# Kernel tuning notes

Measured on AMD Instinct MI355X. Metric: run time of the kernel, lower is better.

## Reference

```python
import jax, jax.numpy as jnp
import numpy as np

ALPHA = 0.2          # leaky relu negative slope
SCALE_ATT = 1.0
NEG_MASK = -9e15


def setup_inputs() -> dict:
    key = jax.random.key(0)
    k1, k2, k3, k4 = jax.random.split(key, 4)
    B, N, Din, Dout = 32, 1024, 256, 256
    h = jax.random.normal(k1, (B, N, Din), dtype=jnp.float32)
    adj = jax.random.randint(k2, (B, N, N), 0, 2, dtype=jnp.int32)
    W = jax.random.normal(k3, (Dout, Din), dtype=jnp.float32) * (1.0 / np.sqrt(Din))
    b = jnp.zeros((Dout,), dtype=jnp.float32)
    a = jax.random.normal(k4, (2 * Dout,), dtype=jnp.float32) * 0.1
    return {"h": h, "adj": adj, "W": W, "b": b, "a": a}


def reference(h, adj, W, b, a):
    # z: [B, N, Dout]
    z = jnp.einsum('bnd,od->bno', h, W) + b
    Dout = z.shape[-1]
    a1, a2 = a[:Dout], a[Dout:]
    # a^T [z_i || z_j] = a1.z_i + a2.z_j  (same math as the N^2 concat)
    s1 = jnp.einsum('bnd,d->bn', z, a1)  # source score per node
    s2 = jnp.einsum('bnd,d->bn', z, a2)  # target score per node
    e = jax.nn.leaky_relu(s1[:, :, None] + s2[:, None, :], negative_slope=ALPHA)
    e = jnp.where(adj > 0, e, NEG_MASK) * SCALE_ATT
    attention = jax.nn.softmax(e, axis=-1)   # [B, N, N]
    # dropout p=0 / eval mode: no-op
    h_prime = jnp.einsum('bij,bjd->bid', attention, z)
    return jax.nn.elu(h_prime)
```

## Files before the change

kernel.cpp:

```cpp
#include <hip/hip_runtime.h>
#include <math.h>

#define LRELU_ALPHA 0.2f
#define NEG_MASK_V -9000000000000000.0f

typedef __attribute__((ext_vector_type(8))) short short8;
typedef __attribute__((ext_vector_type(4))) float floatx4;
typedef __attribute__((ext_vector_type(8))) unsigned short u16x8;
typedef __attribute__((ext_vector_type(4))) unsigned short u16x4;

__device__ __forceinline__ unsigned short f2bf(float x) {
  union { float f; unsigned u; } v; v.f = x;
  unsigned r = v.u + 0x7fff + ((v.u >> 16) & 1);
  return (unsigned short)(r >> 16);
}

__device__ __forceinline__ unsigned cvt_pk_bf16(float lo, float hi) {
  unsigned r;
  asm("v_cvt_pk_bf16_f32 %0, %1, %2" : "=v"(r) : "v"(lo), "v"(hi));
  return r;
}

__global__ __launch_bounds__(256) void prep_kernel(
    const float* __restrict__ W, const float* __restrict__ b,
    const float* __restrict__ a, unsigned short* __restrict__ Wf,
    float* __restrict__ u1, float* __restrict__ u2, float* __restrict__ cst)
{
  const int t = threadIdx.x;
  if (blockIdx.x == 0) {
    float a1s = 0.f, a2s = 0.f;
    #pragma unroll 4
    for (int o = 0; o < 256; ++o) {
      const float w = W[o * 256 + t];
      a1s = fmaf(w, a[o], a1s);
      a2s = fmaf(w, a[256 + o], a2s);
    }
    u1[t] = a1s; u2[t] = a2s;
    if (t < 64) {
      float p1 = 0.f, p2 = 0.f;
      #pragma unroll
      for (int q = 0; q < 4; ++q) {
        const float bv = b[t + q * 64];
        p1 = fmaf(bv, a[t + q * 64], p1);
        p2 = fmaf(bv, a[256 + t + q * 64], p2);
      }
      #pragma unroll
      for (int off = 32; off > 0; off >>= 1) {
        p1 += __shfl_xor(p1, off); p2 += __shfl_xor(p2, off);
      }
      if (t == 0) { cst[0] = p1; cst[1] = p2; }
    }
  } else {
    const int base = (blockIdx.x - 1) * 2048 + t * 8;
    const int o = base >> 8;
    const int k = base & 255;
    const int region = k >> 3;
    const float4 v0 = *(const float4*)&W[base];
    const float4 v1 = *(const float4*)&W[base + 4];
    u16x8 ov;
    ov[0] = f2bf(v0.x); ov[1] = f2bf(v0.y); ov[2] = f2bf(v0.z); ov[3] = f2bf(v0.w);
    ov[4] = f2bf(v1.x); ov[5] = f2bf(v1.y); ov[6] = f2bf(v1.z); ov[7] = f2bf(v1.w);
    *(u16x8*)&Wf[((size_t)region * 256 + o) * 8] = ov;
  }
}

__global__ __launch_bounds__(256) void zmfma_kernel(
    const float* __restrict__ h, const unsigned short* __restrict__ Wf,
    const float* __restrict__ bias, const float* __restrict__ u1,
    const float* __restrict__ u2, const float* __restrict__ cst,
    unsigned short* __restrict__ zf, float* __restrict__ s1,
    float* __restrict__ s2)
{
  __shared__ unsigned short h_tile[2][32][72];

  const int t = threadIdx.x, l = t & 63, w = t >> 6;
  const int g = l >> 4;
  const int bi = blockIdx.x;
  const long row0 = (long)bi * 32;

  floatx4 acc[2][4];
  #pragma unroll
  for (int mf = 0; mf < 2; ++mf)
    #pragma unroll
    for (int nf = 0; nf < 4; ++nf) acc[mf][nf] = (floatx4)0.f;

  float d1a[2] = {0.f, 0.f};
  float d2a[2] = {0.f, 0.f};

  const int srow = t >> 4, scol = (t & 15) * 4;

  {
    const float4 u1v = *(const float4*)&u1[scol];
    const float4 u2v = *(const float4*)&u2[scol];
    #pragma unroll
    for (int p = 0; p < 2; ++p) {
      const float4 hv = *(const float4*)&h[(row0 + p * 16 + srow) * 256 + scol];
      d1a[p] = fmaf(hv.x, u1v.x, fmaf(hv.y, u1v.y, fmaf(hv.z, u1v.z, fmaf(hv.w, u1v.w, d1a[p]))));
      d2a[p] = fmaf(hv.x, u2v.x, fmaf(hv.y, u2v.y, fmaf(hv.z, u2v.z, fmaf(hv.w, u2v.w, d2a[p]))));
      uint2 hb;
      hb.x = cvt_pk_bf16(hv.x, hv.y);
      hb.y = cvt_pk_bf16(hv.z, hv.w);
      *(uint2*)&h_tile[0][p * 16 + srow][scol] = hb;
    }
  }
  __syncthreads();

  #pragma unroll
  for (int s = 0; s < 4; ++s) {
    if (s < 3) {
      const int k0n = (s + 1) * 64;
      const float4 u1v = *(const float4*)&u1[k0n + scol];
      const float4 u2v = *(const float4*)&u2[k0n + scol];
      #pragma unroll
      for (int p = 0; p < 2; ++p) {
        const float4 hv =
            *(const float4*)&h[(row0 + p * 16 + srow) * 256 + k0n + scol];
        d1a[p] = fmaf(hv.x, u1v.x, fmaf(hv.y, u1v.y, fmaf(hv.z, u1v.z, fmaf(hv.w, u1v.w, d1a[p]))));
        d2a[p] = fmaf(hv.x, u2v.x, fmaf(hv.y, u2v.y, fmaf(hv.z, u2v.z, fmaf(hv.w, u2v.w, d2a[p]))));
        uint2 hb;
        hb.x = cvt_pk_bf16(hv.x, hv.y);
        hb.y = cvt_pk_bf16(hv.z, hv.w);
        *(uint2*)&h_tile[(s + 1) & 1][p * 16 + srow][scol] = hb;
      }
    }

    short8 wf[2][4];
    #pragma unroll
    for (int kk = 0; kk < 2; ++kk)
      #pragma unroll
      for (int nf = 0; nf < 4; ++nf)
        wf[kk][nf] = *(const short8*)&Wf[
            ((size_t)(s * 8 + kk * 4 + g) * 256 + w * 64 + nf * 16 + (l & 15)) * 8];

    #pragma unroll
    for (int kk = 0; kk < 2; ++kk) {
      short8 af[2];
      #pragma unroll
      for (int mf = 0; mf < 2; ++mf)
        af[mf] = *(const short8*)&h_tile[s & 1][mf * 16 + (l & 15)][kk * 32 + g * 8];
      #pragma unroll
      for (int nf = 0; nf < 4; ++nf) {
        #pragma unroll
        for (int mf = 0; mf < 2; ++mf)
          acc[mf][nf] = __builtin_amdgcn_mfma_f32_16x16x32_bf16(
              af[mf], wf[kk][nf], acc[mf][nf], 0, 0, 0);
      }
    }
    if (s < 3) __syncthreads();
  }

  {
    const float c1 = cst[0], c2 = cst[1];
    #pragma unroll
    for (int p = 0; p < 2; ++p) {
      float d1 = d1a[p], d2 = d2a[p];
      #pragma unroll
      for (int off = 8; off > 0; off >>= 1) {
        d1 += __shfl_xor(d1, off); d2 += __shfl_xor(d2, off);
      }
      if ((t & 15) == 0) {
        const long row = row0 + p * 16 + srow;
        s1[row] = d1 + c1; s2[row] = d2 + c2;
      }
    }
  }

  #pragma unroll
  for (int nf = 0; nf < 4; ++nf) {
    const int o = w * 64 + nf * 16 + (l & 15);
    const float bv = bias[o];
    #pragma unroll
    for (int mf = 0; mf < 2; ++mf) {
      const int region = (bi & 1) * 4 + mf * 2 + (g >> 1);
      const int jq = (g & 1) * 4;
      uint2 zv;
      zv.x = cvt_pk_bf16(acc[mf][nf][0] + bv, acc[mf][nf][1] + bv);
      zv.y = cvt_pk_bf16(acc[mf][nf][2] + bv, acc[mf][nf][3] + bv);
      *(uint2*)&zf[((size_t)(bi >> 1) * 8 + region) * 2048 + (size_t)o * 8 + jq] = zv;
    }
  }
}

__global__ __launch_bounds__(512, 4) void attn_kernel(
    const unsigned short* __restrict__ zf, const float* __restrict__ s1g,
    const float* __restrict__ s2g, const int* __restrict__ adj,
    float* __restrict__ out)
{
  __shared__ unsigned short p_lds[2][64][72];
  __shared__ float s2s[1024];
  __shared__ float s1s[64];
  __shared__ float sum_lds[64];

  const int t = threadIdx.x;
  const int l = t & 63;
  const int w = t >> 6;

  const int wg = blockIdx.x;
  const int sw = (wg & 7) * 64 + (wg >> 3);
  const int b = sw >> 4;
  const int i0 = (sw & 15) * 64;

  const int i_loc = t >> 3;
  const int jb = (t & 7) * 8;

  const size_t adj_base = (size_t)b * 1024 * 1024 + (size_t)(i0 + i_loc) * 1024 + jb;
  const size_t zf_batch = (size_t)b * 16 * 16384;
  const size_t zf_lane  = (size_t)(l >> 4) * 2048 + (size_t)(w * 32 + (l & 15)) * 8;

  if (t < 64) s1s[t] = s1g[b * 1024 + i0 + t];
  s2s[t] = s2g[b * 1024 + t];
  s2s[512 + t] = s2g[b * 1024 + 512 + t];

  floatx4 acc[4][2];
  #pragma unroll
  for (int mf = 0; mf < 4; ++mf) {
    acc[mf][0] = (floatx4)0.f;
    acc[mf][1] = (floatx4)0.f;
  }
  float sm = 0.f;

  int4 ac0 = *(const int4*)&adj[adj_base];
  int4 ac1 = *(const int4*)&adj[adj_base + 4];

  short8 vz[2][4];
  {
    const unsigned short* zp = zf + zf_batch + zf_lane;
    vz[0][0] = *(const short8*)(zp);
    vz[0][1] = *(const short8*)(zp + 128);
    vz[0][2] = *(const short8*)(zp + 8192);
    vz[0][3] = *(const short8*)(zp + 8320);
  }
  __syncthreads();
  const float s1v = s1s[i_loc];

  for (int jt2 = 0; jt2 < 1024; jt2 += 128) {
    #pragma unroll
    for (int ph = 0; ph < 2; ++ph) {
      const int jt = jt2 + ph * 64;

      const float4 s2a = *(const float4*)&s2s[jt + jb];
      const float4 s2b = *(const float4*)&s2s[jt + jb + 4];
      float e[8] = {s2a.x, s2a.y, s2a.z, s2a.w, s2b.x, s2b.y, s2b.z, s2b.w};
      const int am[8] = {ac0.x, ac0.y, ac0.z, ac0.w, ac1.x, ac1.y, ac1.z, ac1.w};
      #pragma unroll
      for (int q = 0; q < 8; ++q) {
        float x = s1v + e[q];
        x = fmaxf(x, LRELU_ALPHA * x);
        e[q] = am[q] > 0 ? x : NEG_MASK_V;
      }

      if (jt + 64 < 1024) {
        ac0 = *(const int4*)&adj[adj_base + jt + 64];
        ac1 = *(const int4*)&adj[adj_base + jt + 68];
        const unsigned short* zp =
            zf + zf_batch + (size_t)((jt >> 6) + 1) * 16384 + zf_lane;
        vz[ph ^ 1][0] = *(const short8*)(zp);
        vz[ph ^ 1][1] = *(const short8*)(zp + 128);
        vz[ph ^ 1][2] = *(const short8*)(zp + 8192);
        vz[ph ^ 1][3] = *(const short8*)(zp + 8320);
      }

      float p[8];
      #pragma unroll
      for (int q = 0; q < 8; ++q) { p[q] = __expf(e[q]); sm += p[q]; }
      uint4 pk;
      pk.x = cvt_pk_bf16(p[0], p[1]);
      pk.y = cvt_pk_bf16(p[2], p[3]);
      pk.z = cvt_pk_bf16(p[4], p[5]);
      pk.w = cvt_pk_bf16(p[6], p[7]);
      *(uint4*)&p_lds[ph][i_loc][jb] = pk;

      __syncthreads();

      #pragma unroll
      for (int kk = 0; kk < 2; ++kk) {
        #pragma unroll
        for (int mf = 0; mf < 4; ++mf) {
          const short8 af =
              *(const short8*)&p_lds[ph][mf * 16 + (l & 15)][kk * 32 + (l >> 4) * 8];
          acc[mf][0] = __builtin_amdgcn_mfma_f32_16x16x32_bf16(
              af, vz[ph][kk * 2 + 0], acc[mf][0], 0, 0, 0);
          acc[mf][1] = __builtin_amdgcn_mfma_f32_16x16x32_bf16(
              af, vz[ph][kk * 2 + 1], acc[mf][1], 0, 0, 0);
        }
      }
    }
  }

  sm += __shfl_xor(sm, 1);
  sm += __shfl_xor(sm, 2);
  sm += __shfl_xor(sm, 4);
  if ((t & 7) == 0) sum_lds[i_loc] = sm;
  __syncthreads();

  const size_t obase = ((size_t)b * 1024 + i0) * 256 + w * 32;
  #pragma unroll
  for (int mf = 0; mf < 4; ++mf) {
    const int rbase = mf * 16 + ((l >> 4) << 2);
    #pragma unroll
    for (int rg = 0; rg < 4; ++rg) {
      const float inv = 1.0f / sum_lds[rbase + rg];
      #pragma unroll
      for (int nf = 0; nf < 2; ++nf) {
        float v = acc[mf][nf][rg] * inv;
        v = v > 0.f ? v : expm1f(v);
        out[obase + (size_t)(rbase + rg) * 256 + nf * 16 + (l & 15)] = v;
      }
    }
  }
}

extern "C" void kernel_launch(void* const* d_in, const int* in_sizes, int n_in,
                              void* d_out, int out_size, void* d_ws, size_t ws_size,
                              hipStream_t stream) {
  const float* h    = (const float*)d_in[0];
  const int*   adj  = (const int*)d_in[1];
  const float* W    = (const float*)d_in[2];
  const float* bias = (const float*)d_in[3];
  const float* a    = (const float*)d_in[4];
  float* out = (float*)d_out;

  unsigned short* zf = (unsigned short*)d_ws;
  float* s1  = (float*)((char*)d_ws + 16777216);
  float* s2  = (float*)((char*)d_ws + 16908288);
  float* u1  = (float*)((char*)d_ws + 17039360);
  float* u2  = (float*)((char*)d_ws + 17040384);
  float* cst = (float*)((char*)d_ws + 17041408);
  unsigned short* Wf = (unsigned short*)((char*)d_ws + 17825792);

  prep_kernel<<<dim3(33), dim3(256), 0, stream>>>(W, bias, a, Wf, u1, u2, cst);
  zmfma_kernel<<<dim3(1024), dim3(256), 0, stream>>>(h, Wf, bias, u1, u2, cst, zf, s1, s2);
  attn_kernel<<<dim3(512), dim3(512), 0, stream>>>(zf, s1, s2, adj, out);
}
```

Baseline: 68.88 us.

## Precompute adjacency bitmask in separate kernel and read bytes in attention

Adds a streaming kernel that packs the int32 adjacency matrix into one bit per edge. The attention kernel then reads a single mask byte per 8 columns instead of two int4 loads. This moves the heavy adjacency stream out of the compute-bound attention loop into a pure bandwidth kernel and frees registers there. The cost is an extra launch and a small mask write and read, and the two phases no longer overlap.

```diff
diff --git a/kernel.cpp b/kernel.cpp
--- a/kernel.cpp
+++ b/kernel.cpp
@@ -64,6 +64,28 @@
   }
 }
 
+__global__ __launch_bounds__(256) void convert_kernel(
+    const int* __restrict__ adj, unsigned char* __restrict__ msk)
+{
+  const int t = threadIdx.x;
+  const int lane = t & 63;
+  const int wave_id = blockIdx.x * 4 + (t >> 6);
+
+  #pragma unroll
+  for (int it = 0; it < 8; ++it) {
+    const size_t region = (size_t)wave_id * 8 + it;
+    const int* p = adj + region * 512 + lane * 8;
+    const int4 v0 = *(const int4*)(p);
+    const int4 v1 = *(const int4*)(p + 4);
+    unsigned byte =
+        (unsigned)(v0.x > 0)        | ((unsigned)(v0.y > 0) << 1) |
+        ((unsigned)(v0.z > 0) << 2) | ((unsigned)(v0.w > 0) << 3) |
+        ((unsigned)(v1.x > 0) << 4) | ((unsigned)(v1.y > 0) << 5) |
+        ((unsigned)(v1.z > 0) << 6) | ((unsigned)(v1.w > 0) << 7);
+    msk[region * 64 + lane] = (unsigned char)byte;
+  }
+}
+
 __global__ __launch_bounds__(256) void zmfma_kernel(
     const float* __restrict__ h, const unsigned short* __restrict__ Wf,
     const float* __restrict__ bias, const float* __restrict__ u1,
@@ -183,7 +205,7 @@
 
 __global__ __launch_bounds__(512, 4) void attn_kernel(
     const unsigned short* __restrict__ zf, const float* __restrict__ s1g,
-    const float* __restrict__ s2g, const int* __restrict__ adj,
+    const float* __restrict__ s2g, const unsigned char* __restrict__ msk,
     float* __restrict__ out)
 {
   __shared__ unsigned short p_lds[2][64][72];
@@ -203,7 +225,8 @@
   const int i_loc = t >> 3;
   const int jb = (t & 7) * 8;
 
-  const size_t adj_base = (size_t)b * 1024 * 1024 + (size_t)(i0 + i_loc) * 1024 + jb;
+  const unsigned char* mrow =
+      msk + (size_t)(b * 1024 + i0 + i_loc) * 128 + (t & 7);
   const size_t zf_batch = (size_t)b * 16 * 16384;
   const size_t zf_lane  = (size_t)(l >> 4) * 2048 + (size_t)(w * 32 + (l & 15)) * 8;
 
@@ -218,9 +241,6 @@
     acc[mf][1] = (floatx4)0.f;
   }
   float sm = 0.f;
-
-  int4 ac0 = *(const int4*)&adj[adj_base];
-  int4 ac1 = *(const int4*)&adj[adj_base + 4];
 
   short8 vz[2][4];
   {
@@ -238,20 +258,19 @@
     for (int ph = 0; ph < 2; ++ph) {
       const int jt = jt2 + ph * 64;
 
+      const unsigned mbyte = mrow[jt >> 3];
+
       const float4 s2a = *(const float4*)&s2s[jt + jb];
       const float4 s2b = *(const float4*)&s2s[jt + jb + 4];
       float e[8] = {s2a.x, s2a.y, s2a.z, s2a.w, s2b.x, s2b.y, s2b.z, s2b.w};
-      const int am[8] = {ac0.x, ac0.y, ac0.z, ac0.w, ac1.x, ac1.y, ac1.z, ac1.w};
       #pragma unroll
       for (int q = 0; q < 8; ++q) {
         float x = s1v + e[q];
         x = fmaxf(x, LRELU_ALPHA * x);
-        e[q] = am[q] > 0 ? x : NEG_MASK_V;
+        e[q] = (mbyte & (1u << q)) ? x : NEG_MASK_V;
       }
 
       if (jt + 64 < 1024) {
-        ac0 = *(const int4*)&adj[adj_base + jt + 64];
-        ac1 = *(const int4*)&adj[adj_base + jt + 68];
         const unsigned short* zp =
             zf + zf_batch + (size_t)((jt >> 6) + 1) * 16384 + zf_lane;
         vz[ph ^ 1][0] = *(const short8*)(zp);
@@ -327,8 +346,10 @@
   float* u2  = (float*)((char*)d_ws + 17040384);
   float* cst = (float*)((char*)d_ws + 17041408);
   unsigned short* Wf = (unsigned short*)((char*)d_ws + 17825792);
+  unsigned char* msk = (unsigned char*)((char*)d_ws + 20971520);
 
   prep_kernel<<<dim3(33), dim3(256), 0, stream>>>(W, bias, a, Wf, u1, u2, cst);
+  convert_kernel<<<dim3(2048), dim3(256), 0, stream>>>(adj, msk);
   zmfma_kernel<<<dim3(1024), dim3(256), 0, stream>>>(h, Wf, bias, u1, u2, cst, zf, s1, s2);
-  attn_kernel<<<dim3(512), dim3(512), 0, stream>>>(zf, s1, s2, adj, out);
-}
+  attn_kernel<<<dim3(512), dim3(512), 0, stream>>>(zf, s1, s2, msk, out);
+}
```

Result: slower. 86.56 us (+25.7%).
